# Performance work log

Hardware: AMD Instinct MI355X
Metric: run time of the kernel (lower is better)

The kernel has to match this reference:

```python
import jax, jax.numpy as jnp
import numpy as np

BATCH = 262144
N_STEPS = 10  # hard-coded `range(10)` in the original get_cycles


def _euler_to_matrix(e):
    # Standard extrinsic xyz convention: R = Rz(z) @ Ry(y) @ Rx(x)
    x, y, z = e[..., 0], e[..., 1], e[..., 2]
    cx, sx = jnp.cos(x), jnp.sin(x)
    cy, sy = jnp.cos(y), jnp.sin(y)
    cz, sz = jnp.cos(z), jnp.sin(z)
    r0 = jnp.stack([cz * cy, cz * sy * sx - sz * cx, cz * sy * cx + sz * sx], -1)
    r1 = jnp.stack([sz * cy, sz * sy * sx + cz * cx, sz * sy * cx - cz * sx], -1)
    r2 = jnp.stack([-sy, cy * sx, cy * cx], -1)
    return jnp.stack([r0, r1, r2], -2)  # (..., 3, 3)


def _matrix_to_euler(R):
    # Classic rotationMatrixToEulerAngles (inverse of Rz@Ry@Rx), with singular branch
    sy = jnp.sqrt(R[..., 0, 0] ** 2 + R[..., 1, 0] ** 2)
    singular = sy < 1e-6
    x = jnp.where(singular,
                  jnp.arctan2(-R[..., 1, 2], R[..., 1, 1]),
                  jnp.arctan2(R[..., 2, 1], R[..., 2, 2]))
    y = jnp.arctan2(-R[..., 2, 0], sy)
    z = jnp.where(singular, jnp.zeros_like(sy), jnp.arctan2(R[..., 1, 0], R[..., 0, 0]))
    return jnp.stack([x, y, z], -1)


def _get_cycles(x):
    # x: (B, 6*N_STEPS), interleaved [t(3), r(3)] per step (per the original reshape())
    x = jax.lax.stop_gradient(x)  # mirrors .detach().numpy() in the original
    g = x.reshape(x.shape[0], N_STEPS, 6)
    t = g[:, :, :3]   # (B, S, 3) translations
    r = g[:, :, 3:]   # (B, S, 3) euler rotations

    # --- translation part ---
    # The original aliases path_pred[0] onto t[0:3] via .numpy() and mutates it
    # in-place across cycle iterations (j=0 doubles it). The resulting recorded
    # values obey: v_0 = t_0 ; v_i = 2*v_{i-1} + sum_{j=1}^{i-1} t_j
    C = jnp.cumsum(t[:, 1:, :], axis=1)  # C[:, k-1, :] = sum_{j=1..k} t_j
    v = [t[:, 0, :]]
    for i in range(1, N_STEPS):
        tail = C[:, i - 2, :] if i >= 2 else jnp.zeros_like(v[0])
        v.append(2.0 * v[-1] + tail)
    trans = jnp.stack(v, axis=1)  # (B, S, 3)

    # --- rotation part ---
    # numpy `*=` is ELEMENTWISE, so cycle i records
    # matrix_to_euler( R(r_1) * prod_{j<i} R(r_j) )  (Hadamard product)
    R = _euler_to_matrix(r)                    # (B, S, 3, 3)
    CP = jnp.cumprod(R, axis=1)                # CP[:, k] = elemwise prod_{j<=k} R_j
    P = jnp.concatenate([jnp.ones_like(R[:, :1]), CP[:, :-1]], axis=1)  # prod_{j<i}
    M = R[:, 1:2] * P                          # (B, S, 3, 3)
    rot = _matrix_to_euler(M)                  # (B, S, 3)

    return jnp.stack([trans, rot], axis=2)     # (B, S, 2, 3)


def setup_inputs():
    key = jax.random.key(0)
    k1, k2 = jax.random.split(key)
    pred = jax.random.normal(k1, (BATCH, 6 * N_STEPS), dtype=jnp.float32)
    gt = jax.random.normal(k2, (BATCH, 6 * N_STEPS), dtype=jnp.float32)
    return {"pred": pred, "gt": gt}


def reference(pred, gt):
    pred_cycles = _get_cycles(pred)
    gt_cycles = _get_cycles(gt)
    loss = jnp.mean((pred_cycles - gt_cycles) ** 2)
    return loss / BATCH  # original divides the MSE by self.batch_size
```

## Files before the change

kernel.cpp:

```cpp
#include <hip/hip_runtime.h>
#include <math.h>

#define NSTEP 10

__device__ __forceinline__ void euler2mat(float x, float y, float z, float R[9]) {
    float sx, cx, sy, cy, sz, cz;
    __sincosf(x, &sx, &cx);
    __sincosf(y, &sy, &cy);
    __sincosf(z, &sz, &cz);
    R[0] = cz * cy; R[1] = cz * sy * sx - sz * cx; R[2] = cz * sy * cx + sz * sx;
    R[3] = sz * cy; R[4] = sz * sy * sx + cz * cx; R[5] = sz * sy * cx - cz * sx;
    R[6] = -sy;     R[7] = cy * sx;                R[8] = cy * cx;
}

__device__ __forceinline__ void mat2euler(const float M[9], float& ex, float& ey, float& ez) {
    float sy = sqrtf(M[0] * M[0] + M[3] * M[3]);
    bool sing = sy < 1e-6f;
    float a0 = sing ? -M[5] : M[7];
    float a1 = sing ?  M[4] : M[8];
    ex = atan2f(a0, a1);
    ey = atan2f(-M[6], sy);
    ez = sing ? 0.0f : atan2f(M[3], M[0]);
}

__global__ __launch_bounds__(256) void cycle_loss_main(
    const float* __restrict__ pred, const float* __restrict__ gt,
    double* __restrict__ acc_out, int batch)
{
    int idx = blockIdx.x * blockDim.x + threadIdx.x;
    float acc = 0.0f;
    if (idx < batch) {
        float p[60], g[60];
        const float4* p4 = reinterpret_cast<const float4*>(pred) + (size_t)idx * 15;
        const float4* g4 = reinterpret_cast<const float4*>(gt)   + (size_t)idx * 15;
        #pragma unroll
        for (int i = 0; i < 15; ++i) {
            float4 a = p4[i];
            p[4*i+0] = a.x; p[4*i+1] = a.y; p[4*i+2] = a.z; p[4*i+3] = a.w;
            float4 b = g4[i];
            g[4*i+0] = b.x; g[4*i+1] = b.y; g[4*i+2] = b.z; g[4*i+3] = b.w;
        }

        {
            float vp[3], vg[3], cp[3] = {0,0,0}, cg[3] = {0,0,0};
            #pragma unroll
            for (int c = 0; c < 3; ++c) {
                vp[c] = p[c]; vg[c] = g[c];
                float d = vp[c] - vg[c];
                acc += d * d;
            }
            #pragma unroll
            for (int i = 1; i < NSTEP; ++i) {
                #pragma unroll
                for (int c = 0; c < 3; ++c) {
                    if (i >= 2) { cp[c] += p[6*(i-1)+c]; cg[c] += g[6*(i-1)+c]; }
                    vp[c] = 2.0f * vp[c] + cp[c];
                    vg[c] = 2.0f * vg[c] + cg[c];
                    float d = vp[c] - vg[c];
                    acc += d * d;
                }
            }
        }

        {
            float R1p[9], R1g[9];
            euler2mat(p[9],  p[10], p[11], R1p);
            euler2mat(g[9],  g[10], g[11], R1g);
            float Pp[9], Pg[9];
            #pragma unroll
            for (int k = 0; k < 9; ++k) { Pp[k] = 1.0f; Pg[k] = 1.0f; }
            #pragma unroll
            for (int i = 0; i < NSTEP; ++i) {
                float Mp[9], Mg[9];
                #pragma unroll
                for (int k = 0; k < 9; ++k) { Mp[k] = R1p[k] * Pp[k]; Mg[k] = R1g[k] * Pg[k]; }
                float xp, yp, zp, xg, yg, zg;
                mat2euler(Mp, xp, yp, zp);
                mat2euler(Mg, xg, yg, zg);
                float dx = xp - xg, dy = yp - yg, dz = zp - zg;
                acc += dx * dx + dy * dy + dz * dz;
                if (i < NSTEP - 1) {
                    float Rp[9], Rg[9];
                    euler2mat(p[6*i+3], p[6*i+4], p[6*i+5], Rp);
                    euler2mat(g[6*i+3], g[6*i+4], g[6*i+5], Rg);
                    #pragma unroll
                    for (int k = 0; k < 9; ++k) { Pp[k] *= Rp[k]; Pg[k] *= Rg[k]; }
                }
            }
        }
    }

    int lane = threadIdx.x & 63;
    int wid  = threadIdx.x >> 6;
    #pragma unroll
    for (int off = 32; off > 0; off >>= 1)
        acc += __shfl_down(acc, off, 64);
    __shared__ float warp_s[4];
    if (lane == 0) warp_s[wid] = acc;
    __syncthreads();
    if (threadIdx.x == 0) {
        float s = warp_s[0] + warp_s[1] + warp_s[2] + warp_s[3];
        atomicAdd(acc_out, (double)s);
    }
}

__global__ void cycle_loss_fin(const double* __restrict__ acc, float* __restrict__ out, double inv) {
    out[0] = (float)(acc[0] * inv);
}

extern "C" void kernel_launch(void* const* d_in, const int* in_sizes, int n_in,
                              void* d_out, int out_size, void* d_ws, size_t ws_size,
                              hipStream_t stream) {
    const float* pred = (const float*)d_in[0];
    const float* gt   = (const float*)d_in[1];
    int batch = in_sizes[0] / 60;
    double* acc = (double*)d_ws;

    hipMemsetAsync(acc, 0, sizeof(double), stream);

    const int threads = 256;
    const int blocks = (batch + threads - 1) / threads;
    cycle_loss_main<<<blocks, threads, 0, stream>>>(pred, gt, acc, batch);

    double inv = 1.0 / (60.0 * (double)batch * (double)batch);
    cycle_loss_fin<<<1, 1, 0, stream>>>(acc, (float*)d_out, inv);
}
```

Baseline: 152.5 us.

## Stream inputs in chunks, use polynomial atan2, replace atomics with block partials

```diff
diff --git a/kernel.cpp b/kernel.cpp
--- a/kernel.cpp
+++ b/kernel.cpp
@@ -3,88 +3,124 @@
 
 #define NSTEP 10
 
-__device__ __forceinline__ void euler2mat(float x, float y, float z, float R[9]) {
+__device__ __forceinline__ float fast_atan2f(float y, float x) {
+    float ax = fabsf(x), ay = fabsf(y);
+    float mx = fmaxf(ax, ay);
+    float mn = fminf(ax, ay);
+    float a = mn * __builtin_amdgcn_rcpf(fmaxf(mx, 1e-38f));
+    float s = a * a;
+    float r = fmaf(s, fmaf(s, fmaf(s, fmaf(s, 0.0208351f, -0.085133f),
+                                   0.180141f), -0.3302995f), 0.9998660f) * a;
+    if (ay > ax) r = 1.57079632679f - r;
+    if (x < 0.0f) r = 3.14159265359f - r;
+    return copysignf(r, y);
+}
+
+__device__ __forceinline__ void euler2mat(const float e[3], float R[9]) {
     float sx, cx, sy, cy, sz, cz;
-    __sincosf(x, &sx, &cx);
-    __sincosf(y, &sy, &cy);
-    __sincosf(z, &sz, &cz);
+    __sincosf(e[0], &sx, &cx);
+    __sincosf(e[1], &sy, &cy);
+    __sincosf(e[2], &sz, &cz);
     R[0] = cz * cy; R[1] = cz * sy * sx - sz * cx; R[2] = cz * sy * cx + sz * sx;
     R[3] = sz * cy; R[4] = sz * sy * sx + cz * cx; R[5] = sz * sy * cx - cz * sx;
     R[6] = -sy;     R[7] = cy * sx;                R[8] = cy * cx;
 }
 
-__device__ __forceinline__ void mat2euler(const float M[9], float& ex, float& ey, float& ez) {
-    float sy = sqrtf(M[0] * M[0] + M[3] * M[3]);
+__device__ __forceinline__ void mat2euler(const float M[9], float e[3]) {
+    float sy = sqrtf(fmaf(M[0], M[0], M[3] * M[3]));
     bool sing = sy < 1e-6f;
     float a0 = sing ? -M[5] : M[7];
     float a1 = sing ?  M[4] : M[8];
-    ex = atan2f(a0, a1);
-    ey = atan2f(-M[6], sy);
-    ez = sing ? 0.0f : atan2f(M[3], M[0]);
+    e[0] = fast_atan2f(a0, a1);
+    e[1] = fast_atan2f(-M[6], sy);
+    e[2] = sing ? 0.0f : fast_atan2f(M[3], M[0]);
 }
 
-__global__ __launch_bounds__(256) void cycle_loss_main(
+__global__ __launch_bounds__(256, 5) void cycle_loss_main(
     const float* __restrict__ pred, const float* __restrict__ gt,
-    double* __restrict__ acc_out, int batch)
+    float* __restrict__ partial, int batch)
 {
     int idx = blockIdx.x * blockDim.x + threadIdx.x;
     float acc = 0.0f;
     if (idx < batch) {
-        float p[60], g[60];
-        const float4* p4 = reinterpret_cast<const float4*>(pred) + (size_t)idx * 15;
-        const float4* g4 = reinterpret_cast<const float4*>(gt)   + (size_t)idx * 15;
+        const float4* p4 = reinterpret_cast<const float4*>(pred + (size_t)idx * 60);
+        const float4* g4 = reinterpret_cast<const float4*>(gt   + (size_t)idx * 60);
+
+        float vp[3], vg[3], cp[3] = {0,0,0}, cg[3] = {0,0,0}, tpp[3], tpg[3];
+        float Qp[9], Qg[9];
+
         #pragma unroll
-        for (int i = 0; i < 15; ++i) {
-            float4 a = p4[i];
-            p[4*i+0] = a.x; p[4*i+1] = a.y; p[4*i+2] = a.z; p[4*i+3] = a.w;
-            float4 b = g4[i];
-            g[4*i+0] = b.x; g[4*i+1] = b.y; g[4*i+2] = b.z; g[4*i+3] = b.w;
-        }
+        for (int c = 0; c < 5; ++c) {
+            float4 Ap = p4[3*c], Bp = p4[3*c+1], Cp = p4[3*c+2];
+            float4 Ag = g4[3*c], Bg = g4[3*c+1], Cg = g4[3*c+2];
+            float t0p[3] = {Ap.x, Ap.y, Ap.z}, r0p[3] = {Ap.w, Bp.x, Bp.y};
+            float t1p[3] = {Bp.z, Bp.w, Cp.x}, r1p[3] = {Cp.y, Cp.z, Cp.w};
+            float t0g[3] = {Ag.x, Ag.y, Ag.z}, r0g[3] = {Ag.w, Bg.x, Bg.y};
+            float t1g[3] = {Bg.z, Bg.w, Cg.x}, r1g[3] = {Cg.y, Cg.z, Cg.w};
 
-        {
-            float vp[3], vg[3], cp[3] = {0,0,0}, cg[3] = {0,0,0};
-            #pragma unroll
-            for (int c = 0; c < 3; ++c) {
-                vp[c] = p[c]; vg[c] = g[c];
-                float d = vp[c] - vg[c];
-                acc += d * d;
+            if (c == 0) {
+                #pragma unroll
+                for (int k = 0; k < 3; ++k) {
+                    vp[k] = t0p[k]; vg[k] = t0g[k];
+                    float d = vp[k] - vg[k]; acc += d * d;
+                }
+                #pragma unroll
+                for (int k = 0; k < 3; ++k) {
+                    vp[k] *= 2.0f; vg[k] *= 2.0f;
+                    float d = vp[k] - vg[k]; acc += d * d;
+                }
+            } else {
+                #pragma unroll
+                for (int k = 0; k < 3; ++k) {
+                    cp[k] += tpp[k]; cg[k] += tpg[k];
+                    vp[k] = fmaf(2.0f, vp[k], cp[k]);
+                    vg[k] = fmaf(2.0f, vg[k], cg[k]);
+                    float d = vp[k] - vg[k]; acc += d * d;
+                }
+                #pragma unroll
+                for (int k = 0; k < 3; ++k) {
+                    cp[k] += t0p[k]; cg[k] += t0g[k];
+                    vp[k] = fmaf(2.0f, vp[k], cp[k]);
+                    vg[k] = fmaf(2.0f, vg[k], cg[k]);
+                    float d = vp[k] - vg[k]; acc += d * d;
+                }
             }
             #pragma unroll
-            for (int i = 1; i < NSTEP; ++i) {
+            for (int k = 0; k < 3; ++k) { tpp[k] = t1p[k]; tpg[k] = t1g[k]; }
+
+            float ep[3], eg[3];
+            if (c == 0) {
+                euler2mat(r0p, Qp);  euler2mat(r0g, Qg);
+                float Rtp[9], Rtg[9];
+                euler2mat(r1p, Rtp); euler2mat(r1g, Rtg);
+                mat2euler(Rtp, ep);  mat2euler(Rtg, eg);
                 #pragma unroll
-                for (int c = 0; c < 3; ++c) {
-                    if (i >= 2) { cp[c] += p[6*(i-1)+c]; cg[c] += g[6*(i-1)+c]; }
-                    vp[c] = 2.0f * vp[c] + cp[c];
-                    vg[c] = 2.0f * vg[c] + cg[c];
-                    float d = vp[c] - vg[c];
-                    acc += d * d;
+                for (int k = 0; k < 3; ++k) { float d = ep[k] - eg[k]; acc += d * d; }
+                #pragma unroll
+                for (int k = 0; k < 9; ++k) { Qp[k] *= Rtp[k]; Qg[k] *= Rtg[k]; }
+                mat2euler(Qp, ep); mat2euler(Qg, eg);
+                #pragma unroll
+                for (int k = 0; k < 3; ++k) { float d = ep[k] - eg[k]; acc += d * d; }
+                #pragma unroll
+                for (int k = 0; k < 9; ++k) { Qp[k] *= Rtp[k]; Qg[k] *= Rtg[k]; }
+            } else {
+                mat2euler(Qp, ep); mat2euler(Qg, eg);
+                #pragma unroll
+                for (int k = 0; k < 3; ++k) { float d = ep[k] - eg[k]; acc += d * d; }
+                {
+                    float Rtp[9], Rtg[9];
+                    euler2mat(r0p, Rtp); euler2mat(r0g, Rtg);
+                    #pragma unroll
+                    for (int k = 0; k < 9; ++k) { Qp[k] *= Rtp[k]; Qg[k] *= Rtg[k]; }
                 }
-            }
-        }
-
-        {
-            float R1p[9], R1g[9];
-            euler2mat(p[9],  p[10], p[11], R1p);
-            euler2mat(g[9],  g[10], g[11], R1g);
-            float Pp[9], Pg[9];
-            #pragma unroll
-            for (int k = 0; k < 9; ++k) { Pp[k] = 1.0f; Pg[k] = 1.0f; }
-            #pragma unroll
-            for (int i = 0; i < NSTEP; ++i) {
-                float Mp[9], Mg[9];
+                mat2euler(Qp, ep); mat2euler(Qg, eg);
                 #pragma unroll
-                for (int k = 0; k < 9; ++k) { Mp[k] = R1p[k] * Pp[k]; Mg[k] = R1g[k] * Pg[k]; }
-                float xp, yp, zp, xg, yg, zg;
-                mat2euler(Mp, xp, yp, zp);
-                mat2euler(Mg, xg, yg, zg);
-                float dx = xp - xg, dy = yp - yg, dz = zp - zg;
-                acc += dx * dx + dy * dy + dz * dz;
-                if (i < NSTEP - 1) {
-                    float Rp[9], Rg[9];
-                    euler2mat(p[6*i+3], p[6*i+4], p[6*i+5], Rp);
-                    euler2mat(g[6*i+3], g[6*i+4], g[6*i+5], Rg);
+                for (int k = 0; k < 3; ++k) { float d = ep[k] - eg[k]; acc += d * d; }
+                if (c < 4) {
+                    float Rtp[9], Rtg[9];
+                    euler2mat(r1p, Rtp); euler2mat(r1g, Rtg);
                     #pragma unroll
-                    for (int k = 0; k < 9; ++k) { Pp[k] *= Rp[k]; Pg[k] *= Rg[k]; }
+                    for (int k = 0; k < 9; ++k) { Qp[k] *= Rtp[k]; Qg[k] *= Rtg[k]; }
                 }
             }
         }
@@ -98,14 +134,26 @@
     __shared__ float warp_s[4];
     if (lane == 0) warp_s[wid] = acc;
     __syncthreads();
-    if (threadIdx.x == 0) {
-        float s = warp_s[0] + warp_s[1] + warp_s[2] + warp_s[3];
-        atomicAdd(acc_out, (double)s);
-    }
+    if (threadIdx.x == 0)
+        partial[blockIdx.x] = warp_s[0] + warp_s[1] + warp_s[2] + warp_s[3];
 }
 
-__global__ void cycle_loss_fin(const double* __restrict__ acc, float* __restrict__ out, double inv) {
-    out[0] = (float)(acc[0] * inv);
+__global__ __launch_bounds__(256) void cycle_loss_fin(
+    const float* __restrict__ partial, float* __restrict__ out,
+    int nblocks, float inv)
+{
+    int t = threadIdx.x;
+    float s = 0.0f;
+    for (int i = t; i < nblocks; i += 256) s += partial[i];
+    int lane = t & 63, wid = t >> 6;
+    #pragma unroll
+    for (int off = 32; off > 0; off >>= 1)
+        s += __shfl_down(s, off, 64);
+    __shared__ float warp_s[4];
+    if (lane == 0) warp_s[wid] = s;
+    __syncthreads();
+    if (t == 0)
+        out[0] = (warp_s[0] + warp_s[1] + warp_s[2] + warp_s[3]) * inv;
 }
 
 extern "C" void kernel_launch(void* const* d_in, const int* in_sizes, int n_in,
@@ -114,14 +162,12 @@
     const float* pred = (const float*)d_in[0];
     const float* gt   = (const float*)d_in[1];
     int batch = in_sizes[0] / 60;
-    double* acc = (double*)d_ws;
-
-    hipMemsetAsync(acc, 0, sizeof(double), stream);
+    float* partial = (float*)d_ws;
 
     const int threads = 256;
     const int blocks = (batch + threads - 1) / threads;
-    cycle_loss_main<<<blocks, threads, 0, stream>>>(pred, gt, acc, batch);
+    cycle_loss_main<<<blocks, threads, 0, stream>>>(pred, gt, partial, batch);
 
     double inv = 1.0 / (60.0 * (double)batch * (double)batch);
-    cycle_loss_fin<<<1, 1, 0, stream>>>(acc, (float*)d_out, inv);
+    cycle_loss_fin<<<1, threads, 0, stream>>>(partial, (float*)d_out, blocks, (float)inv);
 }
```

New measurement: 256.5 us. +68.2%, slower.
